# Performance work log

Hardware: AMD Instinct MI355X
Metric: run time of the kernel (lower is better)

The kernel has to match this reference:

```python
import jax, jax.numpy as jnp
import numpy as np

H = 64            # hidden_channels
L = 2             # num_layers
E = 300_000       # edges per relation
B = 64            # graphs in batch
NS = [100_000, 20_000, 50_000, 80_000]   # variable, value, operator, constraint
# (src_type, dst_type) for the 9 hetero relations, fixed order
RELS = [(0,1),(0,2),(0,3),(2,3),(3,3),(1,0),(2,0),(3,0),(3,2)]
R = len(RELS)
SLOPE = 0.2       # GATConv leaky_relu negative slope


def setup_inputs() -> dict:
    key = jax.random.key(0)
    ks = iter(jax.random.split(key, 64))
    inp = {}
    for n, N in zip(["x_variable", "x_value", "x_operator", "x_constraint"], NS):
        inp[n] = jax.random.normal(next(ks), (N, H), jnp.float32)
    sc = 1.0 / np.sqrt(H).astype(np.float32)
    inp["Wsrc"] = jax.random.normal(next(ks), (L, R, H, H), jnp.float32) * sc
    inp["Wdst"] = jax.random.normal(next(ks), (L, R, H, H), jnp.float32) * sc
    inp["asrc"] = jax.random.normal(next(ks), (L, R, H), jnp.float32) * sc
    inp["adst"] = jax.random.normal(next(ks), (L, R, H), jnp.float32) * sc
    inp["bias"] = jax.random.normal(next(ks), (L, R, H), jnp.float32) * 0.01
    inp["lin_w"] = jax.random.normal(next(ks), (2, 2 * H), jnp.float32) / np.sqrt(2.0 * H).astype(np.float32)
    inp["lin_b"] = jnp.zeros((2,), jnp.float32)
    for r, (s, d) in enumerate(RELS):
        inp[f"src{r}"] = jax.random.randint(next(ks), (E,), 0, NS[s], jnp.int32)
        inp[f"dst{r}"] = jax.random.randint(next(ks), (E,), 0, NS[d], jnp.int32)
    inp["batch_variable"] = jnp.sort(jax.random.randint(next(ks), (NS[0],), 0, B, jnp.int32))
    inp["batch_constraint"] = jnp.sort(jax.random.randint(next(ks), (NS[3],), 0, B, jnp.int32))
    inp["num_graphs"] = B
    return inp


def _gat(xs, xd, Ws, Wd, a_s, a_d, b, src, dst):
    """Bipartite PyG GATConv (heads=1, add_self_loops=False)."""
    hs = xs @ Ws                         # [Ns, H]
    hd = xd @ Wd                         # [Nd, H]
    al_s = hs @ a_s                      # [Ns]
    al_d = hd @ a_d                      # [Nd]
    score = jax.nn.leaky_relu(al_s[src] + al_d[dst], SLOPE)    # [E]
    nd = xd.shape[0]
    m = jax.ops.segment_max(score, dst, num_segments=nd)
    p = jnp.exp(score - m[dst])
    z = jax.ops.segment_sum(p, dst, num_segments=nd)
    alpha = p / (z[dst] + 1e-16)                               # segment softmax
    out = jax.ops.segment_sum(hs[src] * alpha[:, None], dst, num_segments=nd)
    return out + b


def _seg_mean(x, seg, n):
    s = jax.ops.segment_sum(x, seg, num_segments=n)
    c = jax.ops.segment_sum(jnp.ones((x.shape[0],), x.dtype), seg, num_segments=n)
    return s / jnp.maximum(c, 1.0)[:, None]


def reference(x_variable, x_value, x_operator, x_constraint,
              Wsrc, Wdst, asrc, adst, bias, lin_w, lin_b,
              src0, dst0, src1, dst1, src2, dst2, src3, dst3, src4, dst4,
              src5, dst5, src6, dst6, src7, dst7, src8, dst8,
              batch_variable, batch_constraint, num_graphs):
    xs = [x_variable, x_value, x_operator, x_constraint]
    srcs = [src0, src1, src2, src3, src4, src5, src6, src7, src8]
    dsts = [dst0, dst1, dst2, dst3, dst4, dst5, dst6, dst7, dst8]
    for l in range(L):
        out = [jnp.zeros((x.shape[0], H), x.dtype) for x in xs]
        for r, (s, d) in enumerate(RELS):
            out[d] = out[d] + _gat(xs[s], xs[d], Wsrc[l, r], Wdst[l, r],
                                   asrc[l, r], adst[l, r], bias[l, r],
                                   srcs[r], dsts[r])
        xs = [jax.nn.relu(o) for o in out]   # dropout is identity in eval
    vp = _seg_mean(xs[0], batch_variable, num_graphs)   # [B, H]
    cp = _seg_mean(xs[3], batch_constraint, num_graphs) # [B, H]
    return jnp.concatenate([vp, cp], axis=1) @ lin_w.T + lin_b   # [B, 2]
```

## Files before the change

kernel.cpp:

```cpp
#include <hip/hip_runtime.h>
#include <hip/hip_bf16.h>

#define NH 64
#define NRELS 9
#define NEDGE 300000
#define NGRAPH 64
#define TOTROWS 250000
#define TOTFSEG 660000
#define TOTEDGE (NRELS * NEDGE)
#define NBUCK 977
#define NBC 4
#define CHUNK 2048
#define NBLK ((TOTEDGE + CHUNK - 1) / CHUNK)
#define KCH 20
#define KSP 66
#define BKT_CAP 6144

typedef __attribute__((ext_vector_type(8))) short short8;
typedef __attribute__((ext_vector_type(4))) float f32x4;

__constant__ int c_NS[4]     = {100000, 20000, 50000, 80000};
__constant__ int c_SRC[9]    = {0,0,0,2,3,1,2,3,3};
__constant__ int c_DST[9]    = {1,2,3,3,3,0,0,0,2};
__constant__ int c_XOFF[5]   = {0,100000,120000,170000,250000};
__constant__ int c_ASOFF[10] = {0,100000,200000,300000,350000,430000,450000,500000,580000,660000};
__constant__ int c_FOFF[5]   = {0,300000,320000,420000,660000};
__constant__ int c_NRELT[4]  = {3,1,2,3};
__constant__ int c_RRANK[9]  = {0,0,0,1,2,0,1,2,1};

struct EdgePtrs { const int* s[9]; const int* d[9]; };

__device__ __forceinline__ unsigned short f2bf(float f) {
  union { __hip_bfloat16 h; unsigned short u; } c;
  c.h = __float2bfloat16(f);
  return c.u;
}

__device__ __forceinline__ float wred_max32(float v) {
#pragma unroll
  for (int o = 16; o; o >>= 1) v = fmaxf(v, __shfl_xor(v, o, 32));
  return v;
}
__device__ __forceinline__ float wred_sum32(float v) {
#pragma unroll
  for (int o = 16; o; o >>= 1) v += __shfl_xor(v, o, 32);
  return v;
}

__global__ void k_setup(const float* Wsrc, const float* Wdst, const float* asrc,
                        const float* adst, const float* bias, float* wv, float* bsum) {
  int b = blockIdx.x, j = threadIdx.x;
  if (b < 36) {
    int r = b % 9, q = b / 9;
    int l = q >> 1, side = q & 1;
    const float* W = (side ? Wdst : Wsrc) + (l * 9 + r) * 64 * 64;
    const float* a = (side ? adst : asrc) + (l * 9 + r) * 64;
    float s = 0.f;
    for (int i = 0; i < 64; ++i) s += W[j * 64 + i] * a[i];
    wv[(side ? 1152 : 0) + (l * 9 + r) * 64 + j] = s;
  } else {
    for (int l = 0; l < 2; ++l)
      for (int t = 0; t < 4; ++t) {
        float s = 0.f;
        for (int r = 0; r < 9; ++r)
          if (c_DST[r] == t) s += bias[(l * 9 + r) * 64 + j];
        bsum[(l * 4 + t) * 64 + j] = s;
      }
  }
}

__global__ __launch_bounds__(256) void k_bhist2(EdgePtrs Eg, int* bh) {
  __shared__ int sh[NBUCK];
  for (int i = threadIdx.x; i < NBUCK; i += 256) sh[i] = 0;
  __syncthreads();
  int lo = blockIdx.x * CHUNK;
  int hi = lo + CHUNK; if (hi > TOTEDGE) hi = TOTEDGE;
  for (int gid = lo + threadIdx.x; gid < hi; gid += 256) {
    int r = gid / NEDGE, e = gid - r * NEDGE;
    int g = c_XOFF[c_DST[r]] + Eg.d[r][e];
    atomicAdd(&sh[g >> 8], 1);
  }
  __syncthreads();
  int* dst = bh + (size_t)blockIdx.x * NBUCK;
  for (int i = threadIdx.x; i < NBUCK; i += 256) dst[i] = sh[i];
}

__global__ void k_cs1(const int* bh, int* csum) {
  int blk = blockIdx.x;
  int c = blk / NBC;
  int b = (blk % NBC) * 256 + threadIdx.x;
  if (b >= NBUCK) return;
  int k0 = c * KSP;
  int k1 = k0 + KSP; if (k1 > NBLK) k1 = NBLK;
  int s = 0;
  for (int k = k0; k < k1; ++k) s += bh[(size_t)k * NBUCK + b];
  csum[(size_t)c * NBUCK + b] = s;
}

__global__ void k_cs2(int* csum, int* gbh) {
  int b = blockIdx.x * 256 + threadIdx.x;
  if (b >= NBUCK) return;
  int run = 0;
#pragma unroll
  for (int c = 0; c < KCH; ++c) {
    size_t idx = (size_t)c * NBUCK + b;
    int t = csum[idx];
    csum[idx] = run;
    run += t;
  }
  gbh[b] = run;
}

__global__ void k_cs3(int* bh, const int* csum) {
  int blk = blockIdx.x;
  int c = blk / NBC;
  int b = (blk % NBC) * 256 + threadIdx.x;
  if (b >= NBUCK) return;
  int k0 = c * KSP;
  int k1 = k0 + KSP; if (k1 > NBLK) k1 = NBLK;
  int run = csum[(size_t)c * NBUCK + b];
  for (int k = k0; k < k1; ++k) {
    size_t idx = (size_t)k * NBUCK + b;
    int t = bh[idx];
    bh[idx] = run;
    run += t;
  }
}

__global__ void k_bscan(const int* gbh, int* boff) {
  __shared__ int sd[1024];
  int t = threadIdx.x;
  int v = (t < NBUCK) ? gbh[t] : 0;
  sd[t] = v; __syncthreads();
  for (int o = 1; o < 1024; o <<= 1) {
    int x = (t >= o) ? sd[t - o] : 0; __syncthreads();
    sd[t] += x; __syncthreads();
  }
  if (t < NBUCK) boff[t] = sd[t] - v;
  if (t == 1023) boff[NBUCK] = sd[1023];
}

__global__ __launch_bounds__(256) void k_bin2(EdgePtrs Eg, const int* bh, const int* boff, int* pairs) {
  __shared__ int cur[NBUCK];
  const int* mybh = bh + (size_t)blockIdx.x * NBUCK;
  for (int i = threadIdx.x; i < NBUCK; i += 256) cur[i] = boff[i] + mybh[i];
  __syncthreads();
  int lo = blockIdx.x * CHUNK;
  int hi = lo + CHUNK; if (hi > TOTEDGE) hi = TOTEDGE;
  for (int gid = lo + threadIdx.x; gid < hi; gid += 256) {
    int r = gid / NEDGE, e = gid - r * NEDGE;
    int g = c_XOFF[c_DST[r]] + Eg.d[r][e];
    int b = g >> 8;
    int pos = atomicAdd(&cur[b], 1);
    int key = ((g & 255) << 2) | c_RRANK[r];
    pairs[pos] = (key << 20) | (c_ASOFF[r] + Eg.s[r][e]);
  }
}

__global__ __launch_bounds__(256) void k_bsort(const int* pairs, const int* boff,
                                               int* rowptr, int* asx) {
  __shared__ int spl[BKT_CAP];
  __shared__ int sout[BKT_CAP];
  __shared__ int ssc[1024];
  __shared__ int scur[1024];
  __shared__ int sws[256];
  int b = blockIdx.x, t = threadIdx.x;
  int lo = boff[b], hi = boff[b + 1];
  int n = hi - lo; if (n > BKT_CAP) n = BKT_CAP;
  for (int i = t; i < n; i += 256) spl[i] = pairs[lo + i];
  for (int i = t; i < 1024; i += 256) ssc[i] = 0;
  __syncthreads();
  for (int i = t; i < n; i += 256) atomicAdd(&ssc[((unsigned)spl[i]) >> 20], 1);
  __syncthreads();
  int c0 = ssc[t * 4], c1 = ssc[t * 4 + 1], c2 = ssc[t * 4 + 2], c3 = ssc[t * 4 + 3];
  int s = c0 + c1 + c2 + c3;
  sws[t] = s;
  __syncthreads();
  for (int o = 1; o < 256; o <<= 1) {
    int x = (t >= o) ? sws[t - o] : 0; __syncthreads();
    sws[t] += x; __syncthreads();
  }
  int base = sws[t] - s;
  ssc[t * 4]     = base;
  ssc[t * 4 + 1] = base + c0;
  ssc[t * 4 + 2] = base + c0 + c1;
  ssc[t * 4 + 3] = base + c0 + c1 + c2;
  scur[t * 4]     = ssc[t * 4];
  scur[t * 4 + 1] = ssc[t * 4 + 1];
  scur[t * 4 + 2] = ssc[t * 4 + 2];
  scur[t * 4 + 3] = ssc[t * 4 + 3];
  __syncthreads();
  int nodeBase = b << 8;
  for (int i = t; i < 1024; i += 256) {
    int l = i >> 2, rank = i & 3;
    int g = nodeBase + l;
    if (g < TOTROWS) {
      int tt = (g >= c_XOFF[1]) + (g >= c_XOFF[2]) + (g >= c_XOFF[3]);
      int nr = c_NRELT[tt];
      if (rank < nr)
        rowptr[c_FOFF[tt] + (g - c_XOFF[tt]) * nr + rank] = lo + ssc[i];
    }
  }
  if (b == 0 && t == 0) rowptr[TOTFSEG] = TOTEDGE;
  for (int i = t; i < n; i += 256) {
    int p = spl[i];
    int pos = atomicAdd(&scur[((unsigned)p) >> 20], 1);
    sout[pos] = (int)(((((unsigned)p >> 20) & 3u) << 20) | ((unsigned)p & 0xFFFFFu));
  }
  __syncthreads();
  for (int i = t; i < n; i += 256) asx[lo + i] = sout[i];
}

struct AlphaP {
  const float* x0; const float* x1; const float* x2; const float* x3;
  float* als; float* ald;
  const float* wvs; const float* wvd;
  int act; int smask; int dmask;
};

__global__ __launch_bounds__(256) void k_alphas(AlphaP P) {
  __shared__ float sws[576];
  __shared__ float swd[576];
  for (int i = threadIdx.x; i < 576; i += 256) { sws[i] = P.wvs[i]; swd[i] = P.wvd[i]; }
  __syncthreads();
  int node = blockIdx.x * 256 + threadIdx.x;
  if (node >= TOTROWS) return;
  int t = (node >= c_XOFF[1]) + (node >= c_XOFF[2]) + (node >= c_XOFF[3]);
  int n = node - c_XOFF[t];
  const float* xt = t == 0 ? P.x0 : t == 1 ? P.x1 : t == 2 ? P.x2 : P.x3;
  const float4* rp = (const float4*)xt + (size_t)n * 16;
  float4 row[16];
#pragma unroll
  for (int k = 0; k < 16; ++k) row[k] = rp[k];
  if (P.act) {
#pragma unroll
    for (int k = 0; k < 16; ++k) {
      row[k].x = fmaxf(row[k].x, 0.f); row[k].y = fmaxf(row[k].y, 0.f);
      row[k].z = fmaxf(row[k].z, 0.f); row[k].w = fmaxf(row[k].w, 0.f);
    }
  }
#pragma unroll
  for (int r = 0; r < 9; ++r) {
    bool ns = ((P.smask >> r) & 1) && (c_SRC[r] == t);
    bool nd = ((P.dmask >> r) & 1) && (c_DST[r] == t);
    if (ns) {
      float s = 0.f;
#pragma unroll
      for (int k = 0; k < 16; ++k) {
        float4 w = *(const float4*)&sws[r * 64 + k * 4];
        s += row[k].x * w.x + row[k].y * w.y + row[k].z * w.z + row[k].w * w.w;
      }
      P.als[c_ASOFF[r] + n] = s;
    }
    if (nd) {
      float s = 0.f;
#pragma unroll
      for (int k = 0; k < 16; ++k) {
        float4 w = *(const float4*)&swd[r * 64 + k * 4];
        s += row[k].x * w.x + row[k].y * w.y + row[k].z * w.z + row[k].w * w.w;
      }
      P.ald[c_FOFF[t] + n * c_NRELT[t] + c_RRANK[r]] = s;
    }
  }
}

struct GemmAllP {
  const float* x0; const float* x1; const float* x2; const float* x3;
  const float* Wl;
  __hip_bfloat16* hs;
  int act; int ntyp;
  int tbase[5];
  int typ[4];
  int nrel[4];
  int rel[4][3];
};

#define XSTR 72

__global__ __launch_bounds__(256) void k_gemma(GemmAllP G) {
  __shared__ unsigned short sx[64 * XSTR];
  __shared__ unsigned short sw[64 * XSTR];
  int bid = blockIdx.x;
  int k = 0;
#pragma unroll 3
  for (int q = 1; q < 4; ++q) if (q < G.ntyp) k += (bid >= G.tbase[q]);
  int st = G.typ[k];
  int tile = bid - G.tbase[k];
  int Ns = c_NS[st];
  const float* x = st == 0 ? G.x0 : st == 1 ? G.x1 : st == 2 ? G.x2 : G.x3;
  int base = tile * 64;
  int tid = threadIdx.x;
  for (int kk = tid; kk < 1024; kk += 256) {
    int row = kk >> 4;
    int c4 = (kk & 15) * 4;
    int gr = base + row;
    float4 v = make_float4(0.f, 0.f, 0.f, 0.f);
    if (gr < Ns) v = ((const float4*)x)[(size_t)gr * 16 + (kk & 15)];
    if (G.act) { v.x = fmaxf(v.x, 0.f); v.y = fmaxf(v.y, 0.f); v.z = fmaxf(v.z, 0.f); v.w = fmaxf(v.w, 0.f); }
    ushort4 u;
    u.x = f2bf(v.x); u.y = f2bf(v.y); u.z = f2bf(v.z); u.w = f2bf(v.w);
    *(ushort4*)&sx[row * XSTR + c4] = u;
  }
  __syncthreads();
  int w    = tid >> 6;
  int lane = tid & 63;
  int m    = lane & 15;
  int quad = lane >> 4;
  short8 a0 = *(const short8*)&sx[(w * 16 + m) * XSTR + quad * 8];
  short8 a1 = *(const short8*)&sx[(w * 16 + m) * XSTR + 32 + quad * 8];
  int nrl = G.nrel[k];
  for (int ri = 0; ri < nrl; ++ri) {
    int r = G.rel[k][ri];
    const float* W = G.Wl + r * 4096;
    if (ri) __syncthreads();
    for (int kk = tid; kk < 1024; kk += 256) {
      int krow = kk >> 4;
      int c4 = (kk & 15) * 4;
      float4 v = ((const float4*)W)[kk];
      sw[(c4 + 0) * XSTR + krow] = f2bf(v.x);
      sw[(c4 + 1) * XSTR + krow] = f2bf(v.y);
      sw[(c4 + 2) * XSTR + krow] = f2bf(v.z);
      sw[(c4 + 3) * XSTR + krow] = f2bf(v.w);
    }
    __syncthreads();
    f32x4 acc[4];
#pragma unroll
    for (int cb = 0; cb < 4; ++cb) acc[cb] = (f32x4)(0.f);
#pragma unroll
    for (int cb = 0; cb < 4; ++cb) {
      short8 b0 = *(const short8*)&sw[(cb * 16 + m) * XSTR + quad * 8];
      short8 b1 = *(const short8*)&sw[(cb * 16 + m) * XSTR + 32 + quad * 8];
      acc[cb] = __builtin_amdgcn_mfma_f32_16x16x32_bf16(a0, b0, acc[cb], 0, 0, 0);
      acc[cb] = __builtin_amdgcn_mfma_f32_16x16x32_bf16(a1, b1, acc[cb], 0, 0, 0);
    }
    __hip_bfloat16* hsb = G.hs + (size_t)c_ASOFF[r] * 64;
#pragma unroll
    for (int reg = 0; reg < 4; ++reg) {
      int lr = base + w * 16 + quad * 4 + reg;
      if (lr < Ns) {
#pragma unroll
        for (int cb = 0; cb < 4; ++cb)
          hsb[(size_t)lr * 64 + cb * 16 + m] = __float2bfloat16(acc[cb][reg]);
      }
    }
  }
}

struct GatherAllP {
  const __hip_bfloat16* hs;
  const float* als;
  const float* ald;
  const int* rowptr; const int* asx;
  float* xA;
  const float* bsum;
  int ntypes;
  int tbase[5];
  int typ[4];
};

__global__ __launch_bounds__(256) void k_gatherall(GatherAllP A) {
  __shared__ unsigned long long sRA[8][96];
  int bid = blockIdx.x;
  int k = 0;
#pragma unroll 3
  for (int q = 1; q < 4; ++q) if (q < A.ntypes) k += (bid >= A.tbase[q]);
  int t = A.typ[k];
  int Nd = c_NS[t];
  int lane = threadIdx.x & 63;
  int half = lane >> 5;
  int sl   = lane & 31;
  int hid  = threadIdx.x >> 5;
  int node = (bid - A.tbase[k]) * 8 + (threadIdx.x >> 6) * 2 + half;
  if (node >= Nd) return;
  int nr = c_NRELT[t];
  int fb = c_FOFF[t] + node * nr;
  int p0 = A.rowptr[fb];
  int p1 = A.rowptr[fb + nr];
  int deg = p1 - p0; if (deg > 96) deg = 96;
  float2 acc = ((const float2*)(A.bsum + t * 64))[sl];
  if (deg > 0) {
    const float NEG = -3.4e38f;
    float ald0 = A.ald[fb];
    float ald1 = (nr > 1) ? A.ald[fb + 1] : 0.f;
    float ald2 = (nr > 2) ? A.ald[fb + 2] : 0.f;
    const unsigned* ax = (const unsigned*)A.asx;
    unsigned row0 = 0, row1 = 0, row2 = 0;
    int rk0 = 0, rk1 = 0, rk2 = 0;
    float s0 = NEG, s1 = NEG, s2 = NEG;
    bool ok0 = sl < deg, ok1 = sl + 32 < deg, ok2 = sl + 64 < deg;
    if (ok0) {
      unsigned rec = ax[p0 + sl];
      row0 = rec & 0xFFFFFu; rk0 = (int)((rec >> 20) & 3u);
      float v = A.als[row0] + (rk0 == 0 ? ald0 : (rk0 == 1 ? ald1 : ald2));
      s0 = v >= 0.f ? v : 0.2f * v;
    }
    if (ok1) {
      unsigned rec = ax[p0 + 32 + sl];
      row1 = rec & 0xFFFFFu; rk1 = (int)((rec >> 20) & 3u);
      float v = A.als[row1] + (rk1 == 0 ? ald0 : (rk1 == 1 ? ald1 : ald2));
      s1 = v >= 0.f ? v : 0.2f * v;
    }
    if (ok2) {
      unsigned rec = ax[p0 + 64 + sl];
      row2 = rec & 0xFFFFFu; rk2 = (int)((rec >> 20) & 3u);
      float v = A.als[row2] + (rk2 == 0 ? ald0 : (rk2 == 1 ? ald1 : ald2));
      s2 = v >= 0.f ? v : 0.2f * v;
    }
    float pm0 = fmaxf(fmaxf(rk0 == 0 ? s0 : NEG, rk1 == 0 ? s1 : NEG), rk2 == 0 ? s2 : NEG);
    float pm1 = fmaxf(fmaxf(rk0 == 1 ? s0 : NEG, rk1 == 1 ? s1 : NEG), rk2 == 1 ? s2 : NEG);
    float pm2 = fmaxf(fmaxf(rk0 == 2 ? s0 : NEG, rk1 == 2 ? s1 : NEG), rk2 == 2 ? s2 : NEG);
    float m0 = wred_max32(pm0);
    float m1 = (nr > 1) ? wred_max32(pm1) : NEG;
    float m2 = (nr > 2) ? wred_max32(pm2) : NEG;
    float e0 = ok0 ? __expf(s0 - (rk0 == 0 ? m0 : (rk0 == 1 ? m1 : m2))) : 0.f;
    float e1 = ok1 ? __expf(s1 - (rk1 == 0 ? m0 : (rk1 == 1 ? m1 : m2))) : 0.f;
    float e2 = ok2 ? __expf(s2 - (rk2 == 0 ? m0 : (rk2 == 1 ? m1 : m2))) : 0.f;
    float pz0 = (rk0 == 0 ? e0 : 0.f) + (rk1 == 0 ? e1 : 0.f) + (rk2 == 0 ? e2 : 0.f);
    float pz1 = (rk0 == 1 ? e0 : 0.f) + (rk1 == 1 ? e1 : 0.f) + (rk2 == 1 ? e2 : 0.f);
    float pz2 = (rk0 == 2 ? e0 : 0.f) + (rk1 == 2 ? e1 : 0.f) + (rk2 == 2 ? e2 : 0.f);
    float rz0 = 1.f / (wred_sum32(pz0) + 1e-16f);
    float rz1 = (nr > 1) ? 1.f / (wred_sum32(pz1) + 1e-16f) : 0.f;
    float rz2 = (nr > 2) ? 1.f / (wred_sum32(pz2) + 1e-16f) : 0.f;
    float aa0 = e0 * (rk0 == 0 ? rz0 : (rk0 == 1 ? rz1 : rz2));
    float aa1 = e1 * (rk1 == 0 ? rz0 : (rk1 == 1 ? rz1 : rz2));
    float aa2 = e2 * (rk2 == 0 ? rz0 : (rk2 == 1 ? rz1 : rz2));
    sRA[hid][sl] = ((unsigned long long)__float_as_uint(aa0) << 32) | row0;
    if (deg > 32) sRA[hid][32 + sl] = ((unsigned long long)__float_as_uint(aa1) << 32) | row1;
    if (deg > 64) sRA[hid][64 + sl] = ((unsigned long long)__float_as_uint(aa2) << 32) | row2;
    const unsigned* hsu = (const unsigned*)A.hs;
    int nb = (deg + 7) >> 3;
    for (int b8 = 0; b8 < nb; ++b8) {
      int e0i = b8 << 3;
      unsigned long long ra[8];
#pragma unroll
      for (int q = 0; q < 8; ++q) ra[q] = sRA[hid][e0i + q];
      unsigned h[8];
#pragma unroll
      for (int q = 0; q < 8; ++q)
        h[q] = hsu[(size_t)(unsigned)(ra[q] & 0xFFFFFFFFu) * 32u + (unsigned)sl];
#pragma unroll
      for (int q = 0; q < 8; ++q) {
        float aq = __uint_as_float((unsigned)(ra[q] >> 32));
        acc.x = fmaf(aq, __uint_as_float(h[q] << 16), acc.x);
        acc.y = fmaf(aq, __uint_as_float(h[q] & 0xffff0000u), acc.y);
      }
    }
  }
  float* xout = A.xA + (size_t)c_XOFF[t] * 64;
  *(float2*)&xout[(size_t)node * 64 + sl * 2] = acc;
}

__global__ void k_gbound(const int* bvar, const int* bcon, int* gs0, int* gs3) {
  int gid = blockIdx.x * 256 + threadIdx.x;
  const int N0 = 100000, N3 = 80000;
  if (gid < N0) {
    int i = gid;
    int b = bvar[i];
    int bp = i ? bvar[i - 1] : -1;
    for (int g = bp + 1; g <= b; ++g) gs0[g] = i;
    if (i == N0 - 1) for (int g = b + 1; g <= 64; ++g) gs0[g] = N0;
  } else if (gid < N0 + N3) {
    int i = gid - N0;
    int b = bcon[i];
    int bp = i ? bcon[i - 1] : -1;
    for (int g = bp + 1; g <= b; ++g) gs3[g] = i;
    if (i == N3 - 1) for (int g = b + 1; g <= 64; ++g) gs3[g] = N3;
  }
}

__global__ __launch_bounds__(256) void k_pool2(const float* xfin, const int* gs0, const int* gs3,
                                               float* partial) {
  __shared__ float4 sdv[256];
  int b = blockIdx.x;
  int sp = b >> 7;
  int rem = b & 127;
  int g = rem >> 1;
  int t = rem & 1;
  const int* gs = t ? gs3 : gs0;
  int xbase = t ? 170000 : 0;
  int lo = gs[g], hi = gs[g + 1];
  int len = hi - lo;
  int r0 = lo + (len * sp) / 8;
  int r1 = lo + (len * (sp + 1)) / 8;
  int tid = threadIdx.x;
  int rp = tid >> 4;
  int cq = tid & 15;
  float4 acc = make_float4(0.f, 0.f, 0.f, 0.f);
  for (int row = r0 + rp; row < r1; row += 16) {
    float4 v = ((const float4*)xfin)[(size_t)(xbase + row) * 16 + cq];
    acc.x += fmaxf(v.x, 0.f); acc.y += fmaxf(v.y, 0.f);
    acc.z += fmaxf(v.z, 0.f); acc.w += fmaxf(v.w, 0.f);
  }
  sdv[tid] = acc;
  __syncthreads();
  for (int o = 128; o >= 16; o >>= 1) {
    if (tid < o) {
      float4 a = sdv[tid], c = sdv[tid + o];
      a.x += c.x; a.y += c.y; a.z += c.z; a.w += c.w;
      sdv[tid] = a;
    }
    __syncthreads();
  }
  if (tid < 16) ((float4*)&partial[(size_t)b * 64])[tid] = sdv[tid];
}

__global__ void k_poolred2(const float* partial, float* pool) {
  int g = blockIdx.x >> 1;
  int t = blockIdx.x & 1;
  int col = threadIdx.x;
  float s = 0.f;
#pragma unroll
  for (int sp = 0; sp < 8; ++sp)
    s += partial[(size_t)(((sp << 7) | (g << 1) | t)) * 64 + col];
  pool[(t ? 4096 : 0) + g * 64 + col] = s;
}

__global__ void k_final(const float* pool, const int* gs0, const int* gs3,
                        const float* lin_w, const float* lin_b, float* out) {
  int k = threadIdx.x;
  int g = k >> 1, o = k & 1;
  float c0 = fmaxf((float)(gs0[g + 1] - gs0[g]), 1.f);
  float c3 = fmaxf((float)(gs3[g + 1] - gs3[g]), 1.f);
  float acc = lin_b[o];
  for (int i = 0; i < 64; ++i) {
    acc += (pool[g * 64 + i] / c0) * lin_w[o * 128 + i];
    acc += (pool[4096 + g * 64 + i] / c3) * lin_w[o * 128 + 64 + i];
  }
  out[g * 2 + o] = acc;
}

__global__ void k_bail(float* out) {
  if (threadIdx.x < 128) out[threadIdx.x] = 0.f;
}

extern "C" void kernel_launch(void* const* d_in, const int* in_sizes, int n_in,
                              void* d_out, int out_size, void* d_ws, size_t ws_size,
                              hipStream_t stream) {
  (void)in_sizes; (void)n_in; (void)out_size;
  const size_t O_XA   = 0;
  const size_t O_HS   = 16000000;
  const size_t O_ALS  = 37120000;
  const size_t O_ALD  = 37780000;
  const size_t O_WV   = 39790000;
  const size_t O_BS   = 39792304;
  const size_t O_RP   = 39792816;
  const size_t O_ASX  = 40452832;
  const size_t O_GS   = 43152832;
  const size_t O_PART = 43153088;
  const size_t O_POOL = 43218624;
  const size_t NEED   = 43226816;

  if (ws_size < NEED * 4) {
    k_bail<<<1, 128, 0, stream>>>((float*)d_out);
    return;
  }

  const float* x0 = (const float*)d_in[0];
  const float* x1 = (const float*)d_in[1];
  const float* x2 = (const float*)d_in[2];
  const float* x3 = (const float*)d_in[3];
  const float* Wsrc = (const float*)d_in[4];
  const float* Wdst = (const float*)d_in[5];
  const float* asrc = (const float*)d_in[6];
  const float* adst = (const float*)d_in[7];
  const float* bias = (const float*)d_in[8];
  const float* lin_w = (const float*)d_in[9];
  const float* lin_b = (const float*)d_in[10];
  EdgePtrs Eg;
  for (int r = 0; r < 9; ++r) {
    Eg.s[r] = (const int*)d_in[11 + 2 * r];
    Eg.d[r] = (const int*)d_in[12 + 2 * r];
  }
  const int* bvar = (const int*)d_in[29];
  const int* bcon = (const int*)d_in[30];

  float* ws = (float*)d_ws;
  float* xA   = ws + O_XA;
  __hip_bfloat16* hs = (__hip_bfloat16*)(ws + O_HS);
  int* bh     = (int*)(ws + O_HS);
  int* pairs  = bh + (size_t)NBLK * NBUCK;
  int* gbh    = pairs + 2700000;
  int* boff   = gbh + (NBUCK + 1);
  int* csum   = boff + (NBUCK + 2);
  float* als  = ws + O_ALS;
  float* ald  = ws + O_ALD;
  float* wv   = ws + O_WV;
  float* bsum = ws + O_BS;
  int* rowptr = (int*)(ws + O_RP);
  int* asx    = (int*)(ws + O_ASX);
  int* gs0    = (int*)(ws + O_GS);
  int* gs3    = gs0 + 65;
  float* partial = ws + O_PART;
  float* pool = ws + O_POOL;

  const int h_NS[4]   = {100000, 20000, 50000, 80000};
  const int h_SRC[9]  = {0,0,0,2,3,1,2,3,3};
  const int h_XOFF[4] = {0,100000,120000,170000};

  k_setup<<<37, 64, 0, stream>>>(Wsrc, Wdst, asrc, adst, bias, wv, bsum);

  k_bhist2<<<NBLK, 256, 0, stream>>>(Eg, bh);
  k_cs1<<<KCH * NBC, 256, 0, stream>>>(bh, csum);
  k_cs2<<<NBC, 256, 0, stream>>>(csum, gbh);
  k_cs3<<<KCH * NBC, 256, 0, stream>>>(bh, csum);
  k_bscan<<<1, 1024, 0, stream>>>(gbh, boff);
  k_bin2<<<NBLK, 256, 0, stream>>>(Eg, bh, boff, pairs);
  k_bsort<<<NBUCK, 256, 0, stream>>>(pairs, boff, rowptr, asx);
  k_gbound<<<(180000 + 255) / 256, 256, 0, stream>>>(bvar, bcon, gs0, gs3);

  for (int l = 0; l < 2; ++l) {
    const float* xin[4];
    if (l == 0) { xin[0] = x0; xin[1] = x1; xin[2] = x2; xin[3] = x3; }
    else {
      for (int t = 0; t < 4; ++t) xin[t] = xA + (size_t)h_XOFF[t] * 64;
    }
    int act = (l > 0);
    int relmask = l ? 0x0FC : 0x1FF;

    AlphaP AP;
    AP.x0 = xin[0]; AP.x1 = xin[1]; AP.x2 = xin[2]; AP.x3 = xin[3];
    AP.als = als; AP.ald = ald;
    AP.wvs = wv + l * 576; AP.wvd = wv + 1152 + l * 576;
    AP.act = act; AP.smask = relmask; AP.dmask = relmask;
    k_alphas<<<(TOTROWS + 255) / 256, 256, 0, stream>>>(AP);

    GemmAllP G;
    G.x0 = xin[0]; G.x1 = xin[1]; G.x2 = xin[2]; G.x3 = xin[3];
    G.Wl = Wsrc + (size_t)l * 9 * 4096;
    G.hs = hs; G.act = act;
    int ntyp = 0, cum = 0;
    for (int t = 0; t < 4; ++t) {
      int nr = 0; int rl[3];
      for (int r = 0; r < 9; ++r)
        if (((relmask >> r) & 1) && h_SRC[r] == t) rl[nr++] = r;
      if (!nr) continue;
      G.typ[ntyp] = t; G.nrel[ntyp] = nr;
      for (int i = 0; i < 3; ++i) G.rel[ntyp][i] = (i < nr) ? rl[i] : 0;
      G.tbase[ntyp] = cum;
      cum += (h_NS[t] + 63) / 64;
      ++ntyp;
    }
    G.ntyp = ntyp; G.tbase[ntyp] = cum;
    k_gemma<<<cum, 256, 0, stream>>>(G);

    GatherAllP A;
    A.hs = hs; A.als = als; A.ald = ald;
    A.rowptr = rowptr; A.asx = asx;
    A.xA = xA;
    A.bsum = bsum + l * 256;
    int nt = 0, bcum = 0;
    for (int t = 0; t < 4; ++t) {
      if (l == 1 && (t == 1 || t == 2)) continue;
      A.typ[nt] = t;
      A.tbase[nt] = bcum;
      bcum += (h_NS[t] + 7) / 8;
      ++nt;
    }
    A.ntypes = nt; A.tbase[nt] = bcum;
    k_gatherall<<<bcum, 256, 0, stream>>>(A);
  }

  k_pool2<<<1024, 256, 0, stream>>>(xA, gs0, gs3, partial);
  k_poolred2<<<128, 64, 0, stream>>>(partial, pool);
  k_final<<<1, 128, 0, stream>>>(pool, gs0, gs3, lin_w, lin_b, (float*)d_out);
}
```

Before: 523.8 us.

## Use shared softmax max and LDS atomic sums in gather kernel

The gather kernel now computes one max per destination node across all of its relations instead of a separate max per relation. This is mathematically equivalent for softmax unless the exponentials underflow. The per-relation normalising sums are built with LDS atomics instead of three warp reductions. Row indices are pre-shifted into byte offsets, and the gather loop is unrolled two batches of eight edges deep so more loads are in flight. Together these cut shuffle and select work and expose more memory parallelism, at the cost of LDS atomic contention, reliance on an explicit waitcnt with no barrier, and a small underflow risk when relations have very different score ranges.

```diff
diff --git a/kernel.cpp b/kernel.cpp
--- a/kernel.cpp
+++ b/kernel.cpp
@@ -39,11 +39,6 @@
 __device__ __forceinline__ float wred_max32(float v) {
 #pragma unroll
   for (int o = 16; o; o >>= 1) v = fmaxf(v, __shfl_xor(v, o, 32));
-  return v;
-}
-__device__ __forceinline__ float wred_sum32(float v) {
-#pragma unroll
-  for (int o = 16; o; o >>= 1) v += __shfl_xor(v, o, 32);
   return v;
 }
 
@@ -360,6 +355,7 @@
 
 __global__ __launch_bounds__(256) void k_gatherall(GatherAllP A) {
   __shared__ unsigned long long sRA[8][96];
+  __shared__ float sZ[8][4];
   int bid = blockIdx.x;
   int k = 0;
 #pragma unroll 3
@@ -379,70 +375,81 @@
   int deg = p1 - p0; if (deg > 96) deg = 96;
   float2 acc = ((const float2*)(A.bsum + t * 64))[sl];
   if (deg > 0) {
+    if (sl < 4) sZ[hid][sl] = 0.f;
     const float NEG = -3.4e38f;
-    float ald0 = A.ald[fb];
-    float ald1 = (nr > 1) ? A.ald[fb + 1] : 0.f;
-    float ald2 = (nr > 2) ? A.ald[fb + 2] : 0.f;
     const unsigned* ax = (const unsigned*)A.asx;
-    unsigned row0 = 0, row1 = 0, row2 = 0;
+    unsigned rec0 = 0, rec1 = 0, rec2 = 0;
     int rk0 = 0, rk1 = 0, rk2 = 0;
     float s0 = NEG, s1 = NEG, s2 = NEG;
-    bool ok0 = sl < deg, ok1 = sl + 32 < deg, ok2 = sl + 64 < deg;
-    if (ok0) {
-      unsigned rec = ax[p0 + sl];
-      row0 = rec & 0xFFFFFu; rk0 = (int)((rec >> 20) & 3u);
-      float v = A.als[row0] + (rk0 == 0 ? ald0 : (rk0 == 1 ? ald1 : ald2));
+    if (sl < deg) {
+      rec0 = ax[p0 + sl];
+      rk0 = (int)((rec0 >> 20) & 3u);
+      float v = A.als[rec0 & 0xFFFFFu] + A.ald[fb + rk0];
       s0 = v >= 0.f ? v : 0.2f * v;
     }
-    if (ok1) {
-      unsigned rec = ax[p0 + 32 + sl];
-      row1 = rec & 0xFFFFFu; rk1 = (int)((rec >> 20) & 3u);
-      float v = A.als[row1] + (rk1 == 0 ? ald0 : (rk1 == 1 ? ald1 : ald2));
+    if (sl + 32 < deg) {
+      rec1 = ax[p0 + 32 + sl];
+      rk1 = (int)((rec1 >> 20) & 3u);
+      float v = A.als[rec1 & 0xFFFFFu] + A.ald[fb + rk1];
       s1 = v >= 0.f ? v : 0.2f * v;
     }
-    if (ok2) {
-      unsigned rec = ax[p0 + 64 + sl];
-      row2 = rec & 0xFFFFFu; rk2 = (int)((rec >> 20) & 3u);
-      float v = A.als[row2] + (rk2 == 0 ? ald0 : (rk2 == 1 ? ald1 : ald2));
+    if (sl + 64 < deg) {
+      rec2 = ax[p0 + 64 + sl];
+      rk2 = (int)((rec2 >> 20) & 3u);
+      float v = A.als[rec2 & 0xFFFFFu] + A.ald[fb + rk2];
       s2 = v >= 0.f ? v : 0.2f * v;
     }
-    float pm0 = fmaxf(fmaxf(rk0 == 0 ? s0 : NEG, rk1 == 0 ? s1 : NEG), rk2 == 0 ? s2 : NEG);
-    float pm1 = fmaxf(fmaxf(rk0 == 1 ? s0 : NEG, rk1 == 1 ? s1 : NEG), rk2 == 1 ? s2 : NEG);
-    float pm2 = fmaxf(fmaxf(rk0 == 2 ? s0 : NEG, rk1 == 2 ? s1 : NEG), rk2 == 2 ? s2 : NEG);
-    float m0 = wred_max32(pm0);
-    float m1 = (nr > 1) ? wred_max32(pm1) : NEG;
-    float m2 = (nr > 2) ? wred_max32(pm2) : NEG;
-    float e0 = ok0 ? __expf(s0 - (rk0 == 0 ? m0 : (rk0 == 1 ? m1 : m2))) : 0.f;
-    float e1 = ok1 ? __expf(s1 - (rk1 == 0 ? m0 : (rk1 == 1 ? m1 : m2))) : 0.f;
-    float e2 = ok2 ? __expf(s2 - (rk2 == 0 ? m0 : (rk2 == 1 ? m1 : m2))) : 0.f;
-    float pz0 = (rk0 == 0 ? e0 : 0.f) + (rk1 == 0 ? e1 : 0.f) + (rk2 == 0 ? e2 : 0.f);
-    float pz1 = (rk0 == 1 ? e0 : 0.f) + (rk1 == 1 ? e1 : 0.f) + (rk2 == 1 ? e2 : 0.f);
-    float pz2 = (rk0 == 2 ? e0 : 0.f) + (rk1 == 2 ? e1 : 0.f) + (rk2 == 2 ? e2 : 0.f);
-    float rz0 = 1.f / (wred_sum32(pz0) + 1e-16f);
-    float rz1 = (nr > 1) ? 1.f / (wred_sum32(pz1) + 1e-16f) : 0.f;
-    float rz2 = (nr > 2) ? 1.f / (wred_sum32(pz2) + 1e-16f) : 0.f;
-    float aa0 = e0 * (rk0 == 0 ? rz0 : (rk0 == 1 ? rz1 : rz2));
-    float aa1 = e1 * (rk1 == 0 ? rz0 : (rk1 == 1 ? rz1 : rz2));
-    float aa2 = e2 * (rk2 == 0 ? rz0 : (rk2 == 1 ? rz1 : rz2));
-    sRA[hid][sl] = ((unsigned long long)__float_as_uint(aa0) << 32) | row0;
-    if (deg > 32) sRA[hid][32 + sl] = ((unsigned long long)__float_as_uint(aa1) << 32) | row1;
-    if (deg > 64) sRA[hid][64 + sl] = ((unsigned long long)__float_as_uint(aa2) << 32) | row2;
-    const unsigned* hsu = (const unsigned*)A.hs;
+    float M = wred_max32(fmaxf(fmaxf(s0, s1), s2));
+    float e0 = 0.f, e1 = 0.f, e2 = 0.f;
+    if (sl < deg)      { e0 = __expf(s0 - M); atomicAdd(&sZ[hid][rk0], e0); }
+    if (sl + 32 < deg) { e1 = __expf(s1 - M); atomicAdd(&sZ[hid][rk1], e1); }
+    if (sl + 64 < deg) { e2 = __expf(s2 - M); atomicAdd(&sZ[hid][rk2], e2); }
+    asm volatile("s_waitcnt lgkmcnt(0)" ::: "memory");
+    float rz0 = 1.f / (sZ[hid][0] + 1e-16f);
+    float rz1 = 1.f / (sZ[hid][1] + 1e-16f);
+    float rz2 = 1.f / (sZ[hid][2] + 1e-16f);
+    float a0 = e0 * (rk0 == 0 ? rz0 : (rk0 == 1 ? rz1 : rz2));
+    sRA[hid][sl] = ((unsigned long long)__float_as_uint(a0) << 32) | ((rec0 & 0xFFFFFu) << 7);
+    if (deg > 32) {
+      float a1 = e1 * (rk1 == 0 ? rz0 : (rk1 == 1 ? rz1 : rz2));
+      sRA[hid][32 + sl] = ((unsigned long long)__float_as_uint(a1) << 32) | ((rec1 & 0xFFFFFu) << 7);
+    }
+    if (deg > 64) {
+      float a2 = e2 * (rk2 == 0 ? rz0 : (rk2 == 1 ? rz1 : rz2));
+      sRA[hid][64 + sl] = ((unsigned long long)__float_as_uint(a2) << 32) | ((rec2 & 0xFFFFFu) << 7);
+    }
+    const char* hsb = (const char*)A.hs;
+    unsigned sl4 = (unsigned)sl * 4u;
     int nb = (deg + 7) >> 3;
-    for (int b8 = 0; b8 < nb; ++b8) {
-      int e0i = b8 << 3;
-      unsigned long long ra[8];
-#pragma unroll
-      for (int q = 0; q < 8; ++q) ra[q] = sRA[hid][e0i + q];
-      unsigned h[8];
+    for (int g = 0; g < nb; g += 2) {
+      unsigned long long raA[8], raB[8];
+      unsigned hA[8], hB[8];
+      bool hasB = (g + 1) < nb;
+#pragma unroll
+      for (int q = 0; q < 8; ++q) raA[q] = sRA[hid][g * 8 + q];
 #pragma unroll
       for (int q = 0; q < 8; ++q)
-        h[q] = hsu[(size_t)(unsigned)(ra[q] & 0xFFFFFFFFu) * 32u + (unsigned)sl];
+        hA[q] = *(const unsigned*)(hsb + ((unsigned)(raA[q] & 0xFFFFFFFFu) + sl4));
+      if (hasB) {
+#pragma unroll
+        for (int q = 0; q < 8; ++q) raB[q] = sRA[hid][g * 8 + 8 + q];
+#pragma unroll
+        for (int q = 0; q < 8; ++q)
+          hB[q] = *(const unsigned*)(hsb + ((unsigned)(raB[q] & 0xFFFFFFFFu) + sl4));
+      }
 #pragma unroll
       for (int q = 0; q < 8; ++q) {
-        float aq = __uint_as_float((unsigned)(ra[q] >> 32));
-        acc.x = fmaf(aq, __uint_as_float(h[q] << 16), acc.x);
-        acc.y = fmaf(aq, __uint_as_float(h[q] & 0xffff0000u), acc.y);
+        float aq = __uint_as_float((unsigned)(raA[q] >> 32));
+        acc.x = fmaf(aq, __uint_as_float(hA[q] << 16), acc.x);
+        acc.y = fmaf(aq, __uint_as_float(hA[q] & 0xffff0000u), acc.y);
+      }
+      if (hasB) {
+#pragma unroll
+        for (int q = 0; q < 8; ++q) {
+          float aq = __uint_as_float((unsigned)(raB[q] >> 32));
+          acc.x = fmaf(aq, __uint_as_float(hB[q] << 16), acc.x);
+          acc.y = fmaf(aq, __uint_as_float(hB[q] & 0xffff0000u), acc.y);
+        }
       }
     }
   }
```

Measured after the change: 504.1 us. -3.8%, faster.
